# Kernel optimization log

Measured on AMD Instinct MI355X. Metric: run time of the kernel, lower is better.

## Reference

```python
import jax, jax.numpy as jnp
import numpy as np

HIDDEN = 2048
N_HEADS = 32
N_KV_HEADS = 4
HEAD_DIM = 128
EPS = 1e-6
ROPE_THETA = 1000000.0
B, S = 1, 2048


def setup_inputs() -> dict:
    key = jax.random.key(0)
    ks = jax.random.split(key, 7)
    scale = 0.02
    return {
        "hidden_states": jax.random.normal(ks[0], (B, S, HIDDEN), jnp.float32),
        "wq": jax.random.normal(ks[1], (HIDDEN, N_HEADS * HEAD_DIM), jnp.float32) * scale,
        "wk": jax.random.normal(ks[2], (HIDDEN, N_KV_HEADS * HEAD_DIM), jnp.float32) * scale,
        "wv": jax.random.normal(ks[3], (HIDDEN, N_KV_HEADS * HEAD_DIM), jnp.float32) * scale,
        "wo": jax.random.normal(ks[4], (N_HEADS * HEAD_DIM, HIDDEN), jnp.float32) * scale,
        "q_norm_w": jnp.ones((HEAD_DIM,), jnp.float32),
        "k_norm_w": jnp.ones((HEAD_DIM,), jnp.float32),
    }


def _rmsnorm(x, w, eps=EPS):
    # RMSNorm over last (head_dim) axis, as in Qwen3MoeRMSNorm applied per-head
    var = jnp.mean(jnp.square(x), axis=-1, keepdims=True)
    return x * jax.lax.rsqrt(var + eps) * w


def _rope_cos_sin(seq_len, dtype):
    inv_freq = 1.0 / (ROPE_THETA ** (jnp.arange(0, HEAD_DIM, 2, dtype=jnp.float32) / HEAD_DIM))
    pos = jnp.arange(seq_len, dtype=jnp.float32)
    freqs = pos[:, None] * inv_freq[None, :]          # [S, dh/2]
    emb = jnp.concatenate([freqs, freqs], axis=-1)    # [S, dh]
    return jnp.cos(emb).astype(dtype), jnp.sin(emb).astype(dtype)


def _rotate_half(x):
    h = x.shape[-1] // 2
    return jnp.concatenate([-x[..., h:], x[..., :h]], axis=-1)


def reference(hidden_states, wq, wk, wv, wo, q_norm_w, k_norm_w):
    b, s, _ = hidden_states.shape
    # QKV projections (bias-free)
    q = (hidden_states @ wq).reshape(b, s, N_HEADS, HEAD_DIM)
    k = (hidden_states @ wk).reshape(b, s, N_KV_HEADS, HEAD_DIM)
    v = (hidden_states @ wv).reshape(b, s, N_KV_HEADS, HEAD_DIM)
    # per-head RMSNorm on Q and K
    q = _rmsnorm(q, q_norm_w)
    k = _rmsnorm(k, k_norm_w)
    # RoPE (prefill, start_pos = 0)
    cos, sin = _rope_cos_sin(s, q.dtype)              # [S, dh]
    cos = cos[None, :, None, :]
    sin = sin[None, :, None, :]
    q = q * cos + _rotate_half(q) * sin
    k = k * cos + _rotate_half(k) * sin
    # GQA: repeat KV heads to match Q heads
    groups = N_HEADS // N_KV_HEADS
    k = jnp.repeat(k, groups, axis=2)                 # [B,S,nH,dh]
    v = jnp.repeat(v, groups, axis=2)
    # causal SDPA
    scaling = HEAD_DIM ** -0.5
    scores = jnp.einsum("bqhd,bkhd->bhqk", q, k) * scaling
    causal = jnp.tril(jnp.ones((s, s), dtype=bool))
    scores = jnp.where(causal[None, None], scores, jnp.finfo(scores.dtype).min)
    probs = jax.nn.softmax(scores, axis=-1)
    attn = jnp.einsum("bhqk,bkhd->bqhd", probs, v)    # [B,S,nH,dh]
    attn = attn.reshape(b, s, N_HEADS * HEAD_DIM)
    return attn @ wo
```

## Files before the change

kernel.cpp:

```cpp
#include <hip/hip_runtime.h>
#include <stdint.h>

typedef unsigned short u16;
typedef __bf16 bf16x8 __attribute__((ext_vector_type(8)));
typedef float f32x4 __attribute__((ext_vector_type(4)));
typedef u16 u16x8 __attribute__((ext_vector_type(8)));

#define SEQ 2048
#define QKV_N 5120
#define QN 4096

#if __has_builtin(__builtin_amdgcn_exp2f)
#define EXP2F __builtin_amdgcn_exp2f
#else
#define EXP2F exp2f
#endif

#define QSC (0.08838834764831845f * 1.4426950408889634f)
#define MLOG2E 17.312340490667560f

#define WAIT_VM(n) asm volatile("s_waitcnt vmcnt(" #n ")" ::: "memory")
#define WAIT_LGKM asm volatile("s_waitcnt lgkmcnt(0)" ::: "memory")
#define FENCE asm volatile("" ::: "memory")
#define BARRIER_RAW do { FENCE; __builtin_amdgcn_s_barrier(); FENCE; } while (0)

__device__ __forceinline__ u16 f2bf(float f) {
  union { float f; unsigned u; } v; v.f = f;
  unsigned r = v.u + 0x7fffu + ((v.u >> 16) & 1u);
  return (u16)(r >> 16);
}
__device__ __forceinline__ u16 f2bf_fast(float f) {
  union { float f; unsigned u; } v; v.f = f;
  return (u16)((v.u + 0x8000u) >> 16);
}
__device__ __forceinline__ float bf2f(u16 b) {
  union { unsigned u; float f; } v; v.u = ((unsigned)b) << 16;
  return v.f;
}

__device__ __forceinline__ void gl2lds16(const void* g, void* l) {
  __builtin_amdgcn_global_load_lds((const __attribute__((address_space(1))) void*)g,
                                   (__attribute__((address_space(3))) void*)l, 16, 0, 0);
}

__global__ __launch_bounds__(256) void k_prep(const float* __restrict__ hidden,
                                              const float* __restrict__ wq, const float* __restrict__ wk,
                                              const float* __restrict__ wv, const float* __restrict__ wo,
                                              u16* __restrict__ hid_bf, u16* __restrict__ WT,
                                              u16* __restrict__ woT) {
  __shared__ float t[64][65];
  int bx = blockIdx.x;
  if (bx < 4096) {
    int i = (bx * 256 + threadIdx.x) * 4;
    float4 v = *(const float4*)(hidden + i);
    ushort4 o;
    o.x = f2bf(v.x); o.y = f2bf(v.y); o.z = f2bf(v.z); o.w = f2bf(v.w);
    *(ushort4*)(hid_bf + i) = o;
    return;
  }
  const float* src; u16* dst; int R, C, cx, cy, local;
  if (bx < 4096 + 2048) {
    local = bx - 4096; src = wq; dst = WT; R = 2048; C = 4096;
    cx = local & 63; cy = local >> 6;
  } else if (bx < 4096 + 2048 + 256) {
    local = bx - (4096 + 2048); src = wk; dst = WT + (size_t)4096 * 2048; R = 2048; C = 512;
    cx = local & 7; cy = local >> 3;
  } else if (bx < 4096 + 2048 + 512) {
    local = bx - (4096 + 2048 + 256); src = wv; dst = WT + (size_t)4608 * 2048; R = 2048; C = 512;
    cx = local & 7; cy = local >> 3;
  } else {
    local = bx - (4096 + 2048 + 512); src = wo; dst = woT; R = 4096; C = 2048;
    cx = local & 31; cy = local >> 5;
  }
  const int c0 = cx * 64, r0 = cy * 64;
  {
    int col4 = (threadIdx.x & 15) * 4, row = threadIdx.x >> 4;
#pragma unroll
    for (int p = 0; p < 4; ++p) {
      int r = row + p * 16;
      float4 v = *(const float4*)(src + (size_t)(r0 + r) * C + c0 + col4);
      t[r][col4] = v.x; t[r][col4 + 1] = v.y; t[r][col4 + 2] = v.z; t[r][col4 + 3] = v.w;
    }
  }
  __syncthreads();
  {
    int ch = threadIdx.x & 7, cl = threadIdx.x >> 3;
#pragma unroll
    for (int p = 0; p < 2; ++p) {
      int c = cl + p * 32;
      int rbase = ch * 8;
      u16x8 o;
#pragma unroll
      for (int i = 0; i < 8; ++i) o[i] = f2bf(t[rbase + i][c]);
      *(u16x8*)(dst + (size_t)(c0 + c) * R + r0 + rbase) = o;
    }
  }
}

__global__ __launch_bounds__(256) void k_gemm160(const u16* __restrict__ A, const u16* __restrict__ BT,
                                                 u16* __restrict__ C, int M, int N, int K) {
  __shared__ u16 As[2][128 * 64];
  __shared__ u16 Bs[2][160 * 64];
  const int tid = threadIdx.x;
  const int w = tid >> 6, lane = tid & 63, quad = lane >> 4, l15 = lane & 15;
  const int m0 = blockIdx.y * 128, n0 = blockIdx.x * 160;
  const int mw = (w & 1) * 64, nw = (w >> 1) * 80;

  f32x4 acc[4][5];
#pragma unroll
  for (int i = 0; i < 4; ++i)
#pragma unroll
    for (int j = 0; j < 5; ++j) acc[i][j] = {0.f, 0.f, 0.f, 0.f};

  auto stage = [&](int kt, int buf) {
    const int k0 = kt << 6;
#pragma unroll
    for (int p = 0; p < 4; ++p) {
      int ci = (w * 4 + p) * 64 + lane;
      int row = ci >> 3, gc = (ci & 7) ^ (row & 7);
      gl2lds16(A + (size_t)(m0 + row) * K + k0 + gc * 8, &As[buf][(w * 4 + p) * 512]);
    }
#pragma unroll
    for (int p = 0; p < 5; ++p) {
      int ci = (w * 5 + p) * 64 + lane;
      int row = ci >> 3, gc = (ci & 7) ^ (row & 7);
      gl2lds16(BT + (size_t)(n0 + row) * K + k0 + gc * 8, &Bs[buf][(w * 5 + p) * 512]);
    }
  };

  const int nk = K >> 6;
  stage(0, 0);
  for (int kt = 0; kt < nk; ++kt) {
    WAIT_LGKM;
    BARRIER_RAW;
    if (kt + 1 < nk) {
      stage(kt + 1, (kt + 1) & 1);
      WAIT_VM(9);
    } else {
      WAIT_VM(0);
    }
    BARRIER_RAW;
    const u16* Ac = As[kt & 1];
    const u16* Bc = Bs[kt & 1];
#pragma unroll
    for (int kk = 0; kk < 2; ++kk) {
      bf16x8 a[4], b[5];
#pragma unroll
      for (int mt = 0; mt < 4; ++mt) {
        int row = mw + mt * 16 + l15;
        a[mt] = *(const bf16x8*)(Ac + row * 64 + (((kk * 4 + quad) ^ (row & 7)) * 8));
      }
#pragma unroll
      for (int nt = 0; nt < 5; ++nt) {
        int row = nw + nt * 16 + l15;
        b[nt] = *(const bf16x8*)(Bc + row * 64 + (((kk * 4 + quad) ^ (row & 7)) * 8));
      }
#pragma unroll
      for (int mt = 0; mt < 4; ++mt)
#pragma unroll
        for (int nt = 0; nt < 5; ++nt)
          acc[mt][nt] = __builtin_amdgcn_mfma_f32_16x16x32_bf16(a[mt], b[nt], acc[mt][nt], 0, 0, 0);
    }
  }
#pragma unroll
  for (int mt = 0; mt < 4; ++mt)
#pragma unroll
    for (int nt = 0; nt < 5; ++nt)
#pragma unroll
      for (int r = 0; r < 4; ++r) {
        int row = m0 + mw + mt * 16 + quad * 4 + r;
        int col = n0 + nw + nt * 16 + l15;
        C[(size_t)row * N + col] = f2bf(acc[mt][nt][r]);
      }
}

__global__ __launch_bounds__(256) void k_gemm_sk(const u16* __restrict__ A, const u16* __restrict__ BT,
                                                 float* __restrict__ C, int M, int N, int K) {
  __shared__ u16 As[2][128 * 64];
  __shared__ u16 Bs[2][128 * 64];
  const int tid = threadIdx.x;
  const int w = tid >> 6, lane = tid & 63, quad = lane >> 4, l15 = lane & 15;
  const int m0 = blockIdx.y * 128, n0 = blockIdx.x * 128;
  const int mw = (w & 1) * 64, nw = (w >> 1) * 64;
  const int khalf = K >> 1;
  const int kbase = blockIdx.z * khalf;

  f32x4 acc[4][4];
#pragma unroll
  for (int i = 0; i < 4; ++i)
#pragma unroll
    for (int j = 0; j < 4; ++j) acc[i][j] = {0.f, 0.f, 0.f, 0.f};

  auto stage = [&](int kt, int buf) {
    const int k0 = kbase + (kt << 6);
#pragma unroll
    for (int p = 0; p < 4; ++p) {
      int ci = (w * 4 + p) * 64 + lane;
      int row = ci >> 3, gc = (ci & 7) ^ (row & 7);
      gl2lds16(A + (size_t)(m0 + row) * K + k0 + gc * 8, &As[buf][(w * 4 + p) * 512]);
      gl2lds16(BT + (size_t)(n0 + row) * K + k0 + gc * 8, &Bs[buf][(w * 4 + p) * 512]);
    }
  };

  const int nk = khalf >> 6;
  stage(0, 0);
  for (int kt = 0; kt < nk; ++kt) {
    WAIT_LGKM;
    BARRIER_RAW;
    if (kt + 1 < nk) {
      stage(kt + 1, (kt + 1) & 1);
      WAIT_VM(8);
    } else {
      WAIT_VM(0);
    }
    BARRIER_RAW;
    const u16* Ac = As[kt & 1];
    const u16* Bc = Bs[kt & 1];
#pragma unroll
    for (int kk = 0; kk < 2; ++kk) {
      bf16x8 a[4], b[4];
#pragma unroll
      for (int mt = 0; mt < 4; ++mt) {
        int row = mw + mt * 16 + l15;
        a[mt] = *(const bf16x8*)(Ac + row * 64 + (((kk * 4 + quad) ^ (row & 7)) * 8));
      }
#pragma unroll
      for (int nt = 0; nt < 4; ++nt) {
        int row = nw + nt * 16 + l15;
        b[nt] = *(const bf16x8*)(Bc + row * 64 + (((kk * 4 + quad) ^ (row & 7)) * 8));
      }
#pragma unroll
      for (int mt = 0; mt < 4; ++mt)
#pragma unroll
        for (int nt = 0; nt < 4; ++nt)
          acc[mt][nt] = __builtin_amdgcn_mfma_f32_16x16x32_bf16(a[mt], b[nt], acc[mt][nt], 0, 0, 0);
    }
  }
#pragma unroll
  for (int mt = 0; mt < 4; ++mt)
#pragma unroll
    for (int nt = 0; nt < 4; ++nt)
#pragma unroll
      for (int r = 0; r < 4; ++r) {
        int row = m0 + mw + mt * 16 + quad * 4 + r;
        int col = n0 + nw + nt * 16 + l15;
        atomicAdd(&C[(size_t)row * N + col], acc[mt][nt][r]);
      }
}

__global__ __launch_bounds__(256) void k_post(const u16* __restrict__ QKV,
                                              const float* __restrict__ qw, const float* __restrict__ kw,
                                              u16* __restrict__ qb, u16* __restrict__ kb,
                                              u16* __restrict__ vt) {
  __shared__ u16 t[32][34];
  int bx = blockIdx.x;
  if (bx < 2048) {
    int s = bx;
    int w = threadIdx.x >> 6, lane = threadIdx.x & 63;
    const u16* row = QKV + (size_t)s * QKV_N;
    float inv_freq = EXP2F(-(float)lane * (19.931568569324174f / 64.0f));
    float fr = (float)s * inv_freq;
    float sn, cs;
    __sincosf(fr, &sn, &cs);
    float qw0 = qw[lane], qw1 = qw[lane + 64];
    float kw0 = kw[lane], kw1 = kw[lane + 64];
    for (int item = w; item < 36; item += 4) {
      bool isq = item < 32;
      int h = isq ? item : item - 32;
      int base = isq ? h * 128 : 4096 + h * 128;
      float x0 = bf2f(row[base + lane]), x1 = bf2f(row[base + 64 + lane]);
      float ss = x0 * x0 + x1 * x1;
#pragma unroll
      for (int off = 1; off < 64; off <<= 1) ss += __shfl_xor(ss, off);
      float rr = rsqrtf(ss * (1.0f / 128.0f) + 1e-6f);
      float n0 = x0 * rr * (isq ? qw0 : kw0), n1 = x1 * rr * (isq ? qw1 : kw1);
      float y0 = n0 * cs - n1 * sn;
      float y1 = n1 * cs + n0 * sn;
      if (isq) {
        size_t o = (size_t)s * QN + h * 128 + lane;
        qb[o] = f2bf(y0 * QSC);
        qb[o + 64] = f2bf(y1 * QSC);
      } else {
        size_t o = ((size_t)h * SEQ + s) * 128 + lane;
        kb[o] = f2bf(y0);
        kb[o + 64] = f2bf(y1);
      }
    }
    return;
  }
  int local = bx - 2048;
  int s0 = (local & 63) * 32, d0 = ((local >> 6) & 3) * 32, h = local >> 8;
  int j = threadIdx.x & 31, i0 = threadIdx.x >> 5;
#pragma unroll
  for (int p = 0; p < 4; ++p) {
    int r = i0 + p * 8;
    t[r][j] = QKV[(size_t)(s0 + r) * QKV_N + 4608 + h * 128 + d0 + j];
  }
  __syncthreads();
#pragma unroll
  for (int p = 0; p < 4; ++p) {
    int r = i0 + p * 8;
    vt[((size_t)h * 128 + d0 + r) * SEQ + s0 + j] = t[j][r];
  }
}

__global__ __launch_bounds__(512) void k_flash(const u16* __restrict__ qb_, const u16* __restrict__ kb,
                                               const u16* __restrict__ vt, u16* __restrict__ attn) {
  __shared__ u16 Ks[2][128 * 128];
  __shared__ u16 Vts[128 * 128];
  __shared__ u16 Ps[8][16 * 128];
  const int bx = blockIdx.x;
  const int head = bx & 31;
  const int qblk = 15 - (bx >> 5);
  const int kvh = head >> 3;
  const int q0 = qblk * 128;
  const int tid = threadIdx.x, w = tid >> 6, lane = tid & 63, quad = lane >> 4, l15 = lane & 15;
  const int qrow0 = q0 + w * 16;

  bf16x8 qf[4];
  {
    const u16* qrow = qb_ + (size_t)(qrow0 + l15) * QN + head * 128;
#pragma unroll
    for (int ks = 0; ks < 4; ++ks) qf[ks] = *(const bf16x8*)(qrow + ks * 32 + quad * 8);
  }
  f32x4 o[8];
#pragma unroll
  for (int i = 0; i < 8; ++i) o[i] = {0.f, 0.f, 0.f, 0.f};
  float lr[4] = {0.f, 0.f, 0.f, 0.f};

  const u16* kbase = kb + (size_t)kvh * SEQ * 128;
  const u16* vbase = vt + (size_t)kvh * 128 * SEQ;
  u16* pw = Ps[w];

  auto stageK = [&](int ti, int buf) {
    const int t0 = ti * 128;
#pragma unroll
    for (int p = 0; p < 4; ++p) {
      int ci = (w * 4 + p) * 64 + lane;
      int row = ci >> 4, gc = (ci & 15) ^ (row & 15);
      gl2lds16(kbase + (size_t)(t0 + row) * 128 + gc * 8, &Ks[buf][(w * 4 + p) * 512]);
    }
  };
  auto stageV = [&](int ti) {
    const int t0 = ti * 128;
#pragma unroll
    for (int p = 0; p < 4; ++p) {
      int ci = (w * 4 + p) * 64 + lane;
      int d = ci >> 4, gc = (ci & 15) ^ (d & 15);
      gl2lds16(vbase + (size_t)d * SEQ + t0 + gc * 8, &Vts[(w * 4 + p) * 512]);
    }
  };

  const int nT = qblk + 1;
  stageK(0, 0);
  for (int ti = 0; ti < nT; ++ti) {
    const int t0 = ti * 128;
    const bool more = (ti + 1 < nT);
    WAIT_LGKM;
    BARRIER_RAW;
    if (more) stageK(ti + 1, (ti + 1) & 1);
    stageV(ti);
    if (more) { WAIT_VM(8); } else { WAIT_VM(4); }
    BARRIER_RAW;
    const u16* Kc = Ks[ti & 1];

    f32x4 sa[8];
#pragma unroll
    for (int nt = 0; nt < 8; ++nt) sa[nt] = {0.f, 0.f, 0.f, 0.f};
    __builtin_amdgcn_s_setprio(1);
#pragma unroll
    for (int nt = 0; nt < 8; ++nt) {
      int row = nt * 16 + l15;
#pragma unroll
      for (int ks = 0; ks < 4; ++ks) {
        bf16x8 kf = *(const bf16x8*)(Kc + row * 128 + (((ks * 4 + quad) ^ (row & 15)) * 8));
        sa[nt] = __builtin_amdgcn_mfma_f32_16x16x32_bf16(qf[ks], kf, sa[nt], 0, 0, 0);
      }
    }
    __builtin_amdgcn_s_setprio(0);

    const bool domask = (ti == nT - 1);
#pragma unroll
    for (int nt = 0; nt < 8; ++nt)
#pragma unroll
      for (int r = 0; r < 4; ++r) {
        float p = EXP2F(sa[nt][r] - MLOG2E);
        if (domask) {
          int tcol = t0 + nt * 16 + l15;
          int qr = qrow0 + quad * 4 + r;
          p = (tcol > qr) ? 0.f : p;
        }
        sa[nt][r] = p;
        pw[(quad * 4 + r) * 128 + ((nt ^ quad) << 4) + l15] = f2bf_fast(p);
      }
#pragma unroll
    for (int r = 0; r < 4; ++r)
      lr[r] += ((sa[0][r] + sa[1][r]) + (sa[2][r] + sa[3][r])) +
               ((sa[4][r] + sa[5][r]) + (sa[6][r] + sa[7][r]));

    if (more) { WAIT_VM(4); } else { WAIT_VM(0); }
    BARRIER_RAW;
    WAIT_LGKM;

    __builtin_amdgcn_s_setprio(1);
#pragma unroll
    for (int ks2 = 0; ks2 < 4; ++ks2) {
      int col = (ks2 * 32 + quad * 8) ^ ((l15 & 12) << 2);
      bf16x8 pa = *(const bf16x8*)(pw + l15 * 128 + col);
#pragma unroll
      for (int nt2 = 0; nt2 < 8; ++nt2) {
        int d = nt2 * 16 + l15;
        bf16x8 vf = *(const bf16x8*)(Vts + d * 128 + (((ks2 * 4 + quad) ^ (d & 15)) * 8));
        o[nt2] = __builtin_amdgcn_mfma_f32_16x16x32_bf16(pa, vf, o[nt2], 0, 0, 0);
      }
    }
    __builtin_amdgcn_s_setprio(0);
  }

  float inv[4];
#pragma unroll
  for (int r = 0; r < 4; ++r) {
    float s = lr[r];
    s += __shfl_xor(s, 1);
    s += __shfl_xor(s, 2);
    s += __shfl_xor(s, 4);
    s += __shfl_xor(s, 8);
    inv[r] = 1.0f / s;
  }
#pragma unroll
  for (int nt2 = 0; nt2 < 8; ++nt2)
#pragma unroll
    for (int r = 0; r < 4; ++r) {
      size_t idx = (size_t)(qrow0 + quad * 4 + r) * QN + head * 128 + nt2 * 16 + l15;
      attn[idx] = f2bf_fast(o[nt2][r] * inv[r]);
    }
}

extern "C" void kernel_launch(void* const* d_in, const int* in_sizes, int n_in,
                              void* d_out, int out_size, void* d_ws, size_t ws_size,
                              hipStream_t stream) {
  const float* hidden = (const float*)d_in[0];
  const float* wq = (const float*)d_in[1];
  const float* wk = (const float*)d_in[2];
  const float* wv = (const float*)d_in[3];
  const float* wo = (const float*)d_in[4];
  const float* qnw = (const float*)d_in[5];
  const float* knw = (const float*)d_in[6];
  float* out = (float*)d_out;

  char* ws = (char*)d_ws;
  u16* hid_bf = (u16*)(ws);
  u16* WT = (u16*)(ws + 8388608);
  u16* woT = (u16*)(ws + 29360128);
  u16* QKV = (u16*)(ws + 46137344);
  u16* q_bf = (u16*)(ws + 88080384);
  u16* k_bf = (u16*)(ws + 104857600);
  u16* vt = (u16*)(ws + 106954752);
  u16* attn = (u16*)(ws + 109051904);

  hipMemsetAsync(d_out, 0, (size_t)2048 * 2048 * 4, stream);
  k_prep<<<8704, 256, 0, stream>>>(hidden, wq, wk, wv, wo, hid_bf, WT, woT);
  k_gemm160<<<dim3(32, 16), 256, 0, stream>>>(hid_bf, WT, QKV, 2048, 5120, 2048);
  k_post<<<3072, 256, 0, stream>>>(QKV, qnw, knw, q_bf, k_bf, vt);
  k_flash<<<512, 512, 0, stream>>>(q_bf, k_bf, vt, attn);
  k_gemm_sk<<<dim3(16, 16, 2), 256, 0, stream>>>(attn, woT, out, 2048, 2048, 4096);
}
```

Baseline: 304.9 us.

## Fuse Q RMSNorm and RoPE into flash attention prologue

Moves the per-head Q RMSNorm, RoPE rotation and softmax scaling from the post-processing kernel into the flash-attention kernel's Q fragment load, reading raw Q straight from the QKV buffer. The post kernel now handles only K normalization/RoPE and the V transpose, which avoids writing and re-reading a separate 16 MB bf16 Q buffer. In exchange each flash block recomputes sincos and exp2 for its Q rows in registers, which adds prologue work and register pressure to the attention kernel.

```diff
diff --git a/kernel.cpp b/kernel.cpp
--- a/kernel.cpp
+++ b/kernel.cpp
@@ -249,9 +249,8 @@
 }
 
 __global__ __launch_bounds__(256) void k_post(const u16* __restrict__ QKV,
-                                              const float* __restrict__ qw, const float* __restrict__ kw,
-                                              u16* __restrict__ qb, u16* __restrict__ kb,
-                                              u16* __restrict__ vt) {
+                                              const float* __restrict__ kw,
+                                              u16* __restrict__ kb, u16* __restrict__ vt) {
   __shared__ u16 t[32][34];
   int bx = blockIdx.x;
   if (bx < 2048) {
@@ -262,30 +261,19 @@
     float fr = (float)s * inv_freq;
     float sn, cs;
     __sincosf(fr, &sn, &cs);
-    float qw0 = qw[lane], qw1 = qw[lane + 64];
-    float kw0 = kw[lane], kw1 = kw[lane + 64];
-    for (int item = w; item < 36; item += 4) {
-      bool isq = item < 32;
-      int h = isq ? item : item - 32;
-      int base = isq ? h * 128 : 4096 + h * 128;
-      float x0 = bf2f(row[base + lane]), x1 = bf2f(row[base + 64 + lane]);
-      float ss = x0 * x0 + x1 * x1;
-#pragma unroll
-      for (int off = 1; off < 64; off <<= 1) ss += __shfl_xor(ss, off);
-      float rr = rsqrtf(ss * (1.0f / 128.0f) + 1e-6f);
-      float n0 = x0 * rr * (isq ? qw0 : kw0), n1 = x1 * rr * (isq ? qw1 : kw1);
-      float y0 = n0 * cs - n1 * sn;
-      float y1 = n1 * cs + n0 * sn;
-      if (isq) {
-        size_t o = (size_t)s * QN + h * 128 + lane;
-        qb[o] = f2bf(y0 * QSC);
-        qb[o + 64] = f2bf(y1 * QSC);
-      } else {
-        size_t o = ((size_t)h * SEQ + s) * 128 + lane;
-        kb[o] = f2bf(y0);
-        kb[o + 64] = f2bf(y1);
-      }
-    }
+    int h = w;
+    int base = 4096 + h * 128;
+    float x0 = bf2f(row[base + lane]), x1 = bf2f(row[base + 64 + lane]);
+    float ss = x0 * x0 + x1 * x1;
+#pragma unroll
+    for (int off = 1; off < 64; off <<= 1) ss += __shfl_xor(ss, off);
+    float rr = rsqrtf(ss * (1.0f / 128.0f) + 1e-6f);
+    float n0 = x0 * rr * kw[lane], n1 = x1 * rr * kw[lane + 64];
+    float y0 = n0 * cs - n1 * sn;
+    float y1 = n1 * cs + n0 * sn;
+    size_t o = ((size_t)h * SEQ + s) * 128 + lane;
+    kb[o] = f2bf(y0);
+    kb[o + 64] = f2bf(y1);
     return;
   }
   int local = bx - 2048;
@@ -304,8 +292,10 @@
   }
 }
 
-__global__ __launch_bounds__(512) void k_flash(const u16* __restrict__ qb_, const u16* __restrict__ kb,
-                                               const u16* __restrict__ vt, u16* __restrict__ attn) {
+__global__ __launch_bounds__(512) void k_flash(const u16* __restrict__ QKV, const u16* __restrict__ kb,
+                                               const u16* __restrict__ vt,
+                                               const float* __restrict__ qw,
+                                               u16* __restrict__ attn) {
   __shared__ u16 Ks[2][128 * 128];
   __shared__ u16 Vts[128 * 128];
   __shared__ u16 Ps[8][16 * 128];
@@ -319,10 +309,43 @@
 
   bf16x8 qf[4];
   {
-    const u16* qrow = qb_ + (size_t)(qrow0 + l15) * QN + head * 128;
-#pragma unroll
-    for (int ks = 0; ks < 4; ++ks) qf[ks] = *(const bf16x8*)(qrow + ks * 32 + quad * 8);
-  }
+    const u16* qrow = QKV + (size_t)(qrow0 + l15) * QKV_N + head * 128;
+    float x[4][8];
+    float ss = 0.f;
+#pragma unroll
+    for (int ks = 0; ks < 4; ++ks) {
+      u16x8 raw = *(const u16x8*)(qrow + ks * 32 + quad * 8);
+#pragma unroll
+      for (int j = 0; j < 8; ++j) {
+        float f = bf2f(raw[j]);
+        x[ks][j] = f;
+        ss += f * f;
+      }
+    }
+    ss += __shfl_xor(ss, 16);
+    ss += __shfl_xor(ss, 32);
+    const float rr = rsqrtf(ss * (1.0f / 128.0f) + 1e-6f);
+    const float s_pos = (float)(qrow0 + l15);
+    u16x8 qo[4];
+#pragma unroll
+    for (int ks = 0; ks < 2; ++ks) {
+#pragma unroll
+      for (int j = 0; j < 8; ++j) {
+        int d = ks * 32 + quad * 8 + j;
+        float invf = EXP2F(-(float)d * (19.931568569324174f / 64.0f));
+        float fr = s_pos * invf;
+        float sn, cs;
+        __sincosf(fr, &sn, &cs);
+        float n0 = x[ks][j] * rr * qw[d];
+        float n1 = x[ks + 2][j] * rr * qw[d + 64];
+        qo[ks][j] = f2bf((n0 * cs - n1 * sn) * QSC);
+        qo[ks + 2][j] = f2bf((n1 * cs + n0 * sn) * QSC);
+      }
+    }
+#pragma unroll
+    for (int ks = 0; ks < 4; ++ks) qf[ks] = *(const bf16x8*)&qo[ks];
+  }
+
   f32x4 o[8];
 #pragma unroll
   for (int i = 0; i < 8; ++i) o[i] = {0.f, 0.f, 0.f, 0.f};
@@ -453,7 +476,6 @@
   u16* WT = (u16*)(ws + 8388608);
   u16* woT = (u16*)(ws + 29360128);
   u16* QKV = (u16*)(ws + 46137344);
-  u16* q_bf = (u16*)(ws + 88080384);
   u16* k_bf = (u16*)(ws + 104857600);
   u16* vt = (u16*)(ws + 106954752);
   u16* attn = (u16*)(ws + 109051904);
@@ -461,7 +483,7 @@
   hipMemsetAsync(d_out, 0, (size_t)2048 * 2048 * 4, stream);
   k_prep<<<8704, 256, 0, stream>>>(hidden, wq, wk, wv, wo, hid_bf, WT, woT);
   k_gemm160<<<dim3(32, 16), 256, 0, stream>>>(hid_bf, WT, QKV, 2048, 5120, 2048);
-  k_post<<<3072, 256, 0, stream>>>(QKV, qnw, knw, q_bf, k_bf, vt);
-  k_flash<<<512, 512, 0, stream>>>(q_bf, k_bf, vt, attn);
+  k_post<<<3072, 256, 0, stream>>>(QKV, knw, k_bf, vt);
+  k_flash<<<512, 512, 0, stream>>>(QKV, k_bf, vt, qnw, attn);
   k_gemm_sk<<<dim3(16, 16, 2), 256, 0, stream>>>(attn, woT, out, 2048, 2048, 4096);
 }
```

Measured after the change: 302.4 us. About the same (-0.8%).
